# Kernel optimization log

Measured on AMD Instinct MI355X. Metric: run time of the kernel, lower is better.

## Reference

```python
import jax, jax.numpy as jnp
import numpy as np

HEADS = 16

def setup_inputs() -> dict:
    key = jax.random.key(0)
    ks = jax.random.split(key, 5)
    B, T, D = 4, 2048, 1024
    scale = 0.02
    return {
        "x": jax.random.normal(ks[0], (B, T, D), dtype=jnp.float32),
        "W_attn": jax.random.normal(ks[1], (D, 3 * D), dtype=jnp.float32) * scale,
        "b_attn": jax.random.normal(ks[2], (3 * D,), dtype=jnp.float32) * scale,
        "W_proj": jax.random.normal(ks[3], (D, D), dtype=jnp.float32) * scale,
        "b_proj": jax.random.normal(ks[4], (D,), dtype=jnp.float32) * scale,
    }

def reference(x, W_attn, b_attn, W_proj, b_proj):
    B, T, D = x.shape
    H = HEADS
    hd = D // H
    qkv = x @ W_attn + b_attn                      # [B, T, 3D]
    q, k, v = jnp.split(qkv, 3, axis=2)
    # [B, T, H, hd] -> [B, H, T, hd]
    q = q.reshape(B, T, H, hd).transpose(0, 2, 1, 3)
    k = k.reshape(B, T, H, hd).transpose(0, 2, 1, 3)
    v = v.reshape(B, T, H, hd).transpose(0, 2, 1, 3)
    scale = hd ** 0.5
    scores = jnp.einsum("bhqd,bhkd->bhqk", q, k) / scale
    causal = jnp.tril(jnp.ones((T, T), dtype=bool))
    scores = jnp.where(causal, scores, -jnp.inf)
    attn = jax.nn.softmax(scores, axis=-1)
    out = jnp.einsum("bhqk,bhkd->bhqd", attn, v)    # [B, H, T, hd]
    out = out.transpose(0, 2, 1, 3).reshape(B, T, D)
    return out @ W_proj + b_proj
```

## Files before the change

kernel.cpp:

```cpp
#include <hip/hip_runtime.h>
#include <hip/hip_bf16.h>

using bf16 = __hip_bfloat16;
typedef __attribute__((ext_vector_type(8))) __bf16 bf16x8;
typedef __attribute__((ext_vector_type(4))) short s16x4;
typedef __attribute__((ext_vector_type(4))) float f32x4;

#define B_   4
#define T_   2048
#define D_   1024
#define H_   16
#define HD_  64
#define BH_  (B_ * H_)
#define BT_  (B_ * T_)

#define QSCALE 0.18033688011112042f

__device__ __forceinline__ void gld_lds16(const void* g, void* l) {
    __builtin_amdgcn_global_load_lds(
        (const __attribute__((address_space(1))) unsigned int*)g,
        (__attribute__((address_space(3))) unsigned int*)l,
        16, 0, 0);
}

__device__ __forceinline__ f32x4 mfma16(s16x4 a, s16x4 b, f32x4 c) {
#if defined(__HIP_DEVICE_COMPILE__)
  #if __has_builtin(__builtin_amdgcn_mfma_f32_16x16x16bf16_1k)
    return __builtin_amdgcn_mfma_f32_16x16x16bf16_1k(a, b, c, 0, 0, 0);
  #else
    f32x4 d;
    asm volatile("v_mfma_f32_16x16x16_bf16 %0, %1, %2, %3\n\ts_nop 7\n\ts_nop 7"
                 : "=v"(d) : "v"(a), "v"(b), "v"(c));
    return d;
  #endif
#else
    (void)a; (void)b;
    return c;
#endif
}

__device__ __forceinline__ unsigned bfbits(float x) {
    return (unsigned)__builtin_bit_cast(unsigned short, __float2bfloat16(x));
}

__global__ void cast_kernel(const float* __restrict__ in, bf16* __restrict__ out, int n4) {
    int i = blockIdx.x * 256 + threadIdx.x;
    if (i >= n4) return;
    float4 v = reinterpret_cast<const float4*>(in)[i];
    union { bf16 h[4]; uint2 u; } tmp;
    tmp.h[0] = __float2bfloat16(v.x);
    tmp.h[1] = __float2bfloat16(v.y);
    tmp.h[2] = __float2bfloat16(v.z);
    tmp.h[3] = __float2bfloat16(v.w);
    reinterpret_cast<uint2*>(out)[i] = tmp.u;
}

__global__ void transpose_cast(const float* __restrict__ W, bf16* __restrict__ Wt,
                               int K, int N) {
    __shared__ float tile[32][33];
    int nb = blockIdx.x * 32, kb = blockIdx.y * 32;
    int tx = threadIdx.x, ty = threadIdx.y;
    #pragma unroll
    for (int i = 0; i < 32; i += 8)
        tile[ty + i][tx] = W[(size_t)(kb + ty + i) * N + nb + tx];
    __syncthreads();
    #pragma unroll
    for (int i = 0; i < 32; i += 8)
        Wt[(size_t)(nb + ty + i) * K + kb + tx] = __float2bfloat16(tile[tx][ty + i]);
}

template <int MODE>
__global__ __launch_bounds__(256)
void gemm_bt(const bf16* __restrict__ A, const bf16* __restrict__ Bt,
             const float* __restrict__ bias,
             bf16* __restrict__ Qo, bf16* __restrict__ Ko, bf16* __restrict__ Vo,
             float* __restrict__ Fo) {
    constexpr int K = 1024;
    const int bm = blockIdx.x * 128;
    const int bn = blockIdx.y * 128;
    const int tid  = threadIdx.x;
    const int wid  = tid >> 6;
    const int lane = tid & 63;
    const int wr = (wid >> 1) * 64;
    const int wc = (wid & 1) * 64;
    const int ln_g = lane >> 4;
    const int ln_c = lane & 15;

    __shared__ bf16 sm[3][2][128][32];

    f32x4 acc[4][4] = {};

    const int g_row0 = wid * 32 + (lane >> 2);
    const int g_chk  = ((lane & 3) ^ ((lane >> 3) & 3)) * 8;
    const int l_row0 = wid * 32;
    const int colx = (ln_g * 16) ^ (((ln_c >> 1) & 3) << 4);

#define STAGE(S_, K0_) {                                                              \
    gld_lds16(&A [(size_t)(bm + g_row0)      * K + (K0_) + g_chk], &sm[S_][0][l_row0][0]);      \
    gld_lds16(&A [(size_t)(bm + g_row0 + 16) * K + (K0_) + g_chk], &sm[S_][0][l_row0 + 16][0]); \
    gld_lds16(&Bt[(size_t)(bn + g_row0)      * K + (K0_) + g_chk], &sm[S_][1][l_row0][0]);      \
    gld_lds16(&Bt[(size_t)(bn + g_row0 + 16) * K + (K0_) + g_chk], &sm[S_][1][l_row0 + 16][0]); }

#define COMPUTE(S_) {                                                                    \
    bf16x8 af[4], bfr[4];                                                                \
    _Pragma("unroll")                                                                    \
    for (int m = 0; m < 4; ++m)                                                          \
        af[m] = *reinterpret_cast<const bf16x8*>(                                        \
            (const char*)&sm[S_][0][wr + m * 16 + ln_c][0] + colx);                      \
    _Pragma("unroll")                                                                    \
    for (int n = 0; n < 4; ++n)                                                          \
        bfr[n] = *reinterpret_cast<const bf16x8*>(                                       \
            (const char*)&sm[S_][1][wc + n * 16 + ln_c][0] + colx);                      \
    _Pragma("unroll")                                                                    \
    for (int m = 0; m < 4; ++m)                                                          \
        _Pragma("unroll")                                                                \
        for (int n = 0; n < 4; ++n)                                                      \
            acc[m][n] = __builtin_amdgcn_mfma_f32_16x16x32_bf16(af[m], bfr[n],           \
                                                                 acc[m][n], 0, 0, 0); }

#define WAITV4 { asm volatile("s_waitcnt vmcnt(4) lgkmcnt(0)" ::: "memory");             \
                 __builtin_amdgcn_s_barrier();                                           \
                 __builtin_amdgcn_sched_barrier(0); }
#define WAITV0 { asm volatile("s_waitcnt vmcnt(0) lgkmcnt(0)" ::: "memory");             \
                 __builtin_amdgcn_s_barrier();                                           \
                 __builtin_amdgcn_sched_barrier(0); }

    STAGE(0, 0);
    STAGE(1, 32);

    #pragma unroll 1
    for (int i = 0; i < 10; ++i) {
        const int kb = i * 96;
        WAITV4; STAGE(2, kb + 64);  COMPUTE(0);
        WAITV4; STAGE(0, kb + 96);  COMPUTE(1);
        WAITV4; STAGE(1, kb + 128); COMPUTE(2);
    }
    WAITV4; COMPUTE(0);
    WAITV0; COMPUTE(1);

#undef STAGE
#undef COMPUTE
#undef WAITV4
#undef WAITV0

    #pragma unroll
    for (int m = 0; m < 4; ++m) {
        #pragma unroll
        for (int n = 0; n < 4; ++n) {
            const int col = bn + wc + n * 16 + ln_c;
            const float bcol = bias[col];
            #pragma unroll
            for (int j = 0; j < 4; ++j) {
                const int row = bm + wr + m * 16 + ln_g * 4 + j;
                float v = acc[m][n][j] + bcol;
                if (MODE == 0) {
                    const int part = col >> 10;
                    const int cc = col & 1023;
                    const int h = cc >> 6, d = cc & 63;
                    const int b = row >> 11, t = row & 2047;
                    const int bh = b * H_ + h;
                    if (part == 0)
                        Qo[((size_t)bh * T_ + t) * HD_ + d] = __float2bfloat16(v * QSCALE);
                    else if (part == 1)
                        Ko[((size_t)bh * T_ + t) * HD_ + d] = __float2bfloat16(v);
                    else
                        Vo[((size_t)bh * HD_ + d) * T_ + t] = __float2bfloat16(v);
                } else {
                    Fo[(size_t)row * D_ + col] = v;
                }
            }
        }
    }
}

__global__ __launch_bounds__(256, 4)
void attn_kernel(const bf16* __restrict__ Q, const bf16* __restrict__ K,
                 const bf16* __restrict__ Vt, bf16* __restrict__ ctx) {
    const int bh = blockIdx.x & 63;
    const int qt = 31 - (blockIdx.x >> 6);
    const int tid  = threadIdx.x;
    const int wave = tid >> 6;
    const int lane = tid & 63;
    const int ln_g = lane >> 4;
    const int ln_c = lane & 15;

    const bf16* Qp = Q  + (size_t)bh * T_ * HD_;
    const bf16* Kp = K  + (size_t)bh * T_ * HD_;
    const bf16* Vp = Vt + (size_t)bh * HD_ * T_;

    __shared__ bf16 Ks[64][72];
    __shared__ bf16 Vs[64][72];

    const int srow = tid >> 3;
    const int sc8  = (tid & 7) * 8;

    const int b = bh >> 4, h = bh & 15;

    const int qbase = qt * 64;
    const int qglob = qbase + wave * 16 + ln_c;

    const bf16x8 qf0 = *reinterpret_cast<const bf16x8*>(&Qp[(size_t)qglob * HD_ + ln_g * 8]);
    const bf16x8 qf1 = *reinterpret_cast<const bf16x8*>(&Qp[(size_t)qglob * HD_ + 32 + ln_g * 8]);

    f32x4 o[4] = {};
    float m = -INFINITY, l = 0.f;

    const int nk = qt + 1;

    int4 kr0, kr1, vr0, vr1;
    kr0 = *reinterpret_cast<const int4*>(&Kp[(size_t)srow * HD_ + sc8]);
    kr1 = *reinterpret_cast<const int4*>(&Kp[(size_t)(srow + 32) * HD_ + sc8]);
    vr0 = *reinterpret_cast<const int4*>(&Vp[(size_t)srow * T_ + sc8]);
    vr1 = *reinterpret_cast<const int4*>(&Vp[(size_t)(srow + 32) * T_ + sc8]);
    *reinterpret_cast<int4*>(&Ks[srow][sc8])      = kr0;
    *reinterpret_cast<int4*>(&Ks[srow + 32][sc8]) = kr1;
    *reinterpret_cast<int4*>(&Vs[srow][sc8])      = vr0;
    *reinterpret_cast<int4*>(&Vs[srow + 32][sc8]) = vr1;
    __syncthreads();

    for (int it = 0; it < nk; ++it) {
        const int kb = it * 64;
        const bool notlast = (it + 1 < nk);
        if (notlast) {
            const int kn = kb + 64;
            kr0 = *reinterpret_cast<const int4*>(&Kp[(size_t)(kn + srow) * HD_ + sc8]);
            kr1 = *reinterpret_cast<const int4*>(&Kp[(size_t)(kn + srow + 32) * HD_ + sc8]);
            vr0 = *reinterpret_cast<const int4*>(&Vp[(size_t)srow * T_ + kn + sc8]);
            vr1 = *reinterpret_cast<const int4*>(&Vp[(size_t)(srow + 32) * T_ + kn + sc8]);
        }

        f32x4 st[4];
        __builtin_amdgcn_s_setprio(1);
        #pragma unroll
        for (int kk = 0; kk < 4; ++kk) {
            bf16x8 kfa = *reinterpret_cast<const bf16x8*>(&Ks[kk * 16 + ln_c][ln_g * 8]);
            bf16x8 kfb = *reinterpret_cast<const bf16x8*>(&Ks[kk * 16 + ln_c][32 + ln_g * 8]);
            f32x4 z = {0.f, 0.f, 0.f, 0.f};
            z = __builtin_amdgcn_mfma_f32_16x16x32_bf16(kfa, qf0, z, 0, 0, 0);
            z = __builtin_amdgcn_mfma_f32_16x16x32_bf16(kfb, qf1, z, 0, 0, 0);
            st[kk] = z;
        }
        __builtin_amdgcn_s_setprio(0);

        if (!notlast) {
            #pragma unroll
            for (int kk = 0; kk < 4; ++kk)
                #pragma unroll
                for (int j = 0; j < 4; ++j)
                    if (kb + kk * 16 + ln_g * 4 + j > qglob) st[kk][j] = -INFINITY;
        }

        float mx = -INFINITY;
        #pragma unroll
        for (int kk = 0; kk < 4; ++kk)
            #pragma unroll
            for (int j = 0; j < 4; ++j)
                mx = fmaxf(mx, st[kk][j]);
        if (!__all(mx - m <= 8.f)) {
            float r = fmaxf(mx, __shfl_xor(mx, 16));
            r = fmaxf(r, __shfl_xor(r, 32));
            const float mnew = fmaxf(m, r);
            const float alpha = exp2f(m - mnew);
            l *= alpha;
            #pragma unroll
            for (int dt = 0; dt < 4; ++dt)
                #pragma unroll
                for (int j = 0; j < 4; ++j)
                    o[dt][j] *= alpha;
            m = mnew;
        }

        #pragma unroll
        for (int kk = 0; kk < 4; ++kk) {
            float p0 = exp2f(st[kk][0] - m);
            float p1 = exp2f(st[kk][1] - m);
            float p2 = exp2f(st[kk][2] - m);
            float p3 = exp2f(st[kk][3] - m);
            l += (p0 + p1) + (p2 + p3);
            uint2 pw;
            pw.x = bfbits(p0) | (bfbits(p1) << 16);
            pw.y = bfbits(p2) | (bfbits(p3) << 16);
            const s16x4 ps = __builtin_bit_cast(s16x4, pw);
            __builtin_amdgcn_s_setprio(1);
            #pragma unroll
            for (int dt = 0; dt < 4; ++dt) {
                s16x4 vf = *reinterpret_cast<const s16x4*>(
                    &Vs[dt * 16 + ln_c][kk * 16 + ln_g * 4]);
                o[dt] = mfma16(vf, ps, o[dt]);
            }
            __builtin_amdgcn_s_setprio(0);
        }

        if (notlast) {
            __syncthreads();
            *reinterpret_cast<int4*>(&Ks[srow][sc8])      = kr0;
            *reinterpret_cast<int4*>(&Ks[srow + 32][sc8]) = kr1;
            *reinterpret_cast<int4*>(&Vs[srow][sc8])      = vr0;
            *reinterpret_cast<int4*>(&Vs[srow + 32][sc8]) = vr1;
            __syncthreads();
        }
    }

    l += __shfl_xor(l, 16);
    l += __shfl_xor(l, 32);
    const float inv = 1.0f / l;
    bf16* dst = ctx + ((size_t)(b * T_ + qglob)) * D_ + h * HD_;
    #pragma unroll
    for (int dt = 0; dt < 4; ++dt) {
        union { bf16 hh[4]; uint2 u; } ok;
        #pragma unroll
        for (int j = 0; j < 4; ++j)
            ok.hh[j] = __float2bfloat16(o[dt][j] * inv);
        *reinterpret_cast<uint2*>(&dst[dt * 16 + ln_g * 4]) = ok.u;
    }
}

extern "C" void kernel_launch(void* const* d_in, const int* in_sizes, int n_in,
                              void* d_out, int out_size, void* d_ws, size_t ws_size,
                              hipStream_t stream) {
    const float* x      = (const float*)d_in[0];
    const float* W_attn = (const float*)d_in[1];
    const float* b_attn = (const float*)d_in[2];
    const float* W_proj = (const float*)d_in[3];
    const float* b_proj = (const float*)d_in[4];
    float* out = (float*)d_out;

    char* ws = (char*)d_ws;
    bf16* xh  = (bf16*)ws;  ws += (size_t)BT_ * D_ * 2;
    bf16* WaT = (bf16*)ws;  ws += (size_t)3 * D_ * D_ * 2;
    bf16* WpT = (bf16*)ws;  ws += (size_t)D_ * D_ * 2;
    bf16* Qb  = (bf16*)ws;  ws += (size_t)BH_ * T_ * HD_ * 2;
    bf16* Kb  = (bf16*)ws;  ws += (size_t)BH_ * T_ * HD_ * 2;
    bf16* Vb  = (bf16*)ws;  ws += (size_t)BH_ * T_ * HD_ * 2;
    bf16* ctx = (bf16*)ws;  ws += (size_t)BT_ * D_ * 2;

    cast_kernel<<<(BT_ * D_ / 4 + 255) / 256, 256, 0, stream>>>(x, xh, BT_ * D_ / 4);
    transpose_cast<<<dim3(3 * D_ / 32, D_ / 32), dim3(32, 8), 0, stream>>>(W_attn, WaT, D_, 3 * D_);
    transpose_cast<<<dim3(D_ / 32, D_ / 32), dim3(32, 8), 0, stream>>>(W_proj, WpT, D_, D_);

    gemm_bt<0><<<dim3(BT_ / 128, 3 * D_ / 128), 256, 0, stream>>>(
        xh, WaT, b_attn, Qb, Kb, Vb, nullptr);

    attn_kernel<<<dim3(BH_ * 32), 256, 0, stream>>>(Qb, Kb, Vb, ctx);

    gemm_bt<1><<<dim3(BT_ / 128, D_ / 128), 256, 0, stream>>>(
        ctx, WpT, b_proj, nullptr, nullptr, nullptr, out);
}
```

Baseline: 186.2 us.

## Load GEMM A operand directly from global into registers, stage only B in LDS

The GEMM main loop stops staging the A tile through shared memory. Each wave now loads its A fragments straight from global memory into registers, double-buffered across iterations, while only B goes through a 4-deep LDS ring. The aim is to cut LDS traffic, LDS reads and shared-memory footprint, which could raise occupancy. In exchange, A rows are read from global with non-coalesced 16-byte strided loads, and the two column-waves load the same A rows twice, adding L2 traffic and extra register pressure.

```diff
diff --git a/kernel.cpp b/kernel.cpp
--- a/kernel.cpp
+++ b/kernel.cpp
@@ -86,7 +86,7 @@
     const int ln_g = lane >> 4;
     const int ln_c = lane & 15;
 
-    __shared__ bf16 sm[3][2][128][32];
+    __shared__ bf16 smB[4][128][32];
 
     f32x4 acc[4][4] = {};
 
@@ -95,53 +95,59 @@
     const int l_row0 = wid * 32;
     const int colx = (ln_g * 16) ^ (((ln_c >> 1) & 3) << 4);
 
-#define STAGE(S_, K0_) {                                                              \
-    gld_lds16(&A [(size_t)(bm + g_row0)      * K + (K0_) + g_chk], &sm[S_][0][l_row0][0]);      \
-    gld_lds16(&A [(size_t)(bm + g_row0 + 16) * K + (K0_) + g_chk], &sm[S_][0][l_row0 + 16][0]); \
-    gld_lds16(&Bt[(size_t)(bn + g_row0)      * K + (K0_) + g_chk], &sm[S_][1][l_row0][0]);      \
-    gld_lds16(&Bt[(size_t)(bn + g_row0 + 16) * K + (K0_) + g_chk], &sm[S_][1][l_row0 + 16][0]); }
-
-#define COMPUTE(S_) {                                                                    \
-    bf16x8 af[4], bfr[4];                                                                \
+    const bf16* Arow = A + (size_t)(bm + wr + ln_c) * K + ln_g * 8;
+
+#define LOADA(R_, T_) {                                                                  \
     _Pragma("unroll")                                                                    \
     for (int m = 0; m < 4; ++m)                                                          \
-        af[m] = *reinterpret_cast<const bf16x8*>(                                        \
-            (const char*)&sm[S_][0][wr + m * 16 + ln_c][0] + colx);                      \
+        R_[m] = *reinterpret_cast<const bf16x8*>(&Arow[(size_t)m * 16 * K + (T_) * 32]); }
+
+#define STAGEB(S_, T_) {                                                                 \
+    gld_lds16(&Bt[(size_t)(bn + g_row0)      * K + (T_) * 32 + g_chk], &smB[S_][l_row0][0]);      \
+    gld_lds16(&Bt[(size_t)(bn + g_row0 + 16) * K + (T_) * 32 + g_chk], &smB[S_][l_row0 + 16][0]); }
+
+#define COMPUTE(S_, AF_) {                                                               \
+    bf16x8 bfr[4];                                                                       \
     _Pragma("unroll")                                                                    \
     for (int n = 0; n < 4; ++n)                                                          \
         bfr[n] = *reinterpret_cast<const bf16x8*>(                                       \
-            (const char*)&sm[S_][1][wc + n * 16 + ln_c][0] + colx);                      \
+            (const char*)&smB[S_][wc + n * 16 + ln_c][0] + colx);                        \
     _Pragma("unroll")                                                                    \
     for (int m = 0; m < 4; ++m)                                                          \
         _Pragma("unroll")                                                                \
         for (int n = 0; n < 4; ++n)                                                      \
-            acc[m][n] = __builtin_amdgcn_mfma_f32_16x16x32_bf16(af[m], bfr[n],           \
+            acc[m][n] = __builtin_amdgcn_mfma_f32_16x16x32_bf16(AF_[m], bfr[n],          \
                                                                  acc[m][n], 0, 0, 0); }
 
-#define WAITV4 { asm volatile("s_waitcnt vmcnt(4) lgkmcnt(0)" ::: "memory");             \
-                 __builtin_amdgcn_s_barrier();                                           \
-                 __builtin_amdgcn_sched_barrier(0); }
-#define WAITV0 { asm volatile("s_waitcnt vmcnt(0) lgkmcnt(0)" ::: "memory");             \
-                 __builtin_amdgcn_s_barrier();                                           \
-                 __builtin_amdgcn_sched_barrier(0); }
-
-    STAGE(0, 0);
-    STAGE(1, 32);
+#define WAITV(N_) { asm volatile("s_waitcnt vmcnt(" #N_ ") lgkmcnt(0)" ::: "memory");    \
+                    __builtin_amdgcn_s_barrier();                                        \
+                    __builtin_amdgcn_sched_barrier(0); }
+
+    bf16x8 afA[4], afB[4];
+
+    STAGEB(0, 0);
+    STAGEB(1, 1);
+    STAGEB(2, 2);
+    LOADA(afA, 0);
+    WAITV(0);
 
     #pragma unroll 1
-    for (int i = 0; i < 10; ++i) {
-        const int kb = i * 96;
-        WAITV4; STAGE(2, kb + 64);  COMPUTE(0);
-        WAITV4; STAGE(0, kb + 96);  COMPUTE(1);
-        WAITV4; STAGE(1, kb + 128); COMPUTE(2);
+    for (int i = 0; i < 7; ++i) {
+        const int t0 = i * 4;
+        LOADA(afB, t0 + 1); STAGEB((t0 + 3) & 3, t0 + 3); COMPUTE((t0 + 0) & 3, afA); WAITV(2);
+        LOADA(afA, t0 + 2); STAGEB((t0 + 4) & 3, t0 + 4); COMPUTE((t0 + 1) & 3, afB); WAITV(2);
+        LOADA(afB, t0 + 3); STAGEB((t0 + 5) & 3, t0 + 5); COMPUTE((t0 + 2) & 3, afA); WAITV(2);
+        LOADA(afA, t0 + 4); STAGEB((t0 + 6) & 3, t0 + 6); COMPUTE((t0 + 3) & 3, afB); WAITV(2);
     }
-    WAITV4; COMPUTE(0);
-    WAITV0; COMPUTE(1);
-
-#undef STAGE
+    LOADA(afB, 29); STAGEB(3, 31); COMPUTE(0, afA); WAITV(2);
+    LOADA(afA, 30);                COMPUTE(1, afB); WAITV(0);
+    LOADA(afB, 31);                COMPUTE(2, afA); WAITV(0);
+                                   COMPUTE(3, afB);
+
+#undef LOADA
+#undef STAGEB
 #undef COMPUTE
-#undef WAITV4
-#undef WAITV0
+#undef WAITV
 
     #pragma unroll
     for (int m = 0; m < 4; ++m) {
```

New measurement: 254.4 us. 1.37x slower.

## Use 256x256 tiles with 8 waves for the QKV projection GEMM

Applied to the files above, without the earlier changes.

Adds a dedicated QKV GEMM kernel that uses 256x256 output tiles, 512 threads and 96KB of dynamic LDS, with each wave computing a 128x64 sub-tile. The larger tile raises the arithmetic intensity per LDS byte and reduces global reloads of A and B compared with 128x128 tiles. The output projection keeps the old kernel with the template split out. In exchange the grid drops to 384 blocks, which risks poorer occupancy and wave quantization across the CUs, and the doubled accumulator count raises register pressure.

```diff
diff --git a/kernel.cpp b/kernel.cpp
--- a/kernel.cpp
+++ b/kernel.cpp
@@ -69,12 +69,107 @@
         Wt[(size_t)(nb + ty + i) * K + kb + tx] = __float2bfloat16(tile[tx][ty + i]);
 }
 
-template <int MODE>
+__global__ __launch_bounds__(512, 2)
+void gemm_qkv256(const bf16* __restrict__ A, const bf16* __restrict__ Bt,
+                 const float* __restrict__ bias,
+                 bf16* __restrict__ Qo, bf16* __restrict__ Ko, bf16* __restrict__ Vo) {
+    constexpr int K = 1024;
+    extern __shared__ char smem[];
+    const int bm = blockIdx.x * 256;
+    const int bn = blockIdx.y * 256;
+    const int tid  = threadIdx.x;
+    const int wid  = tid >> 6;
+    const int lane = tid & 63;
+    const int wr = (wid >> 2) * 128;
+    const int wc = (wid & 3) * 64;
+    const int ln_g = lane >> 4;
+    const int ln_c = lane & 15;
+
+    f32x4 acc[8][4] = {};
+
+    const int s_row = wid * 16 + (lane >> 2);
+    const int g_chk = ((lane & 3) ^ ((lane >> 3) & 3)) * 8;
+    const int l_off = wid * 1024;
+
+    const int colx = (ln_g * 16) ^ (((ln_c >> 1) & 3) << 4);
+    const char* aB = smem + (wr + ln_c) * 64 + colx;
+    const char* bB = smem + 16384 + (wc + ln_c) * 64 + colx;
+
+#define STAGE(S_, T_) {                                                                   \
+    gld_lds16(&A [(size_t)(bm + s_row)       * K + (T_) * 32 + g_chk], smem + (S_)*32768 + l_off);          \
+    gld_lds16(&A [(size_t)(bm + 128 + s_row) * K + (T_) * 32 + g_chk], smem + (S_)*32768 + 8192 + l_off);   \
+    gld_lds16(&Bt[(size_t)(bn + s_row)       * K + (T_) * 32 + g_chk], smem + (S_)*32768 + 16384 + l_off);  \
+    gld_lds16(&Bt[(size_t)(bn + 128 + s_row) * K + (T_) * 32 + g_chk], smem + (S_)*32768 + 24576 + l_off); }
+
+#define COMPUTE(S_) {                                                                    \
+    bf16x8 af[8], bfr[4];                                                                \
+    _Pragma("unroll")                                                                    \
+    for (int m = 0; m < 8; ++m)                                                          \
+        af[m] = *reinterpret_cast<const bf16x8*>(aB + (S_) * 32768 + m * 1024);          \
+    _Pragma("unroll")                                                                    \
+    for (int n = 0; n < 4; ++n)                                                          \
+        bfr[n] = *reinterpret_cast<const bf16x8*>(bB + (S_) * 32768 + n * 1024);         \
+    _Pragma("unroll")                                                                    \
+    for (int m = 0; m < 8; ++m)                                                          \
+        _Pragma("unroll")                                                                \
+        for (int n = 0; n < 4; ++n)                                                      \
+            acc[m][n] = __builtin_amdgcn_mfma_f32_16x16x32_bf16(af[m], bfr[n],           \
+                                                                 acc[m][n], 0, 0, 0); }
+
+#define WAITV4 { asm volatile("s_waitcnt vmcnt(4) lgkmcnt(0)" ::: "memory");             \
+                 __builtin_amdgcn_s_barrier();                                           \
+                 __builtin_amdgcn_sched_barrier(0); }
+#define WAITV0 { asm volatile("s_waitcnt vmcnt(0) lgkmcnt(0)" ::: "memory");             \
+                 __builtin_amdgcn_s_barrier();                                           \
+                 __builtin_amdgcn_sched_barrier(0); }
+
+    STAGE(0, 0);
+    STAGE(1, 1);
+
+    #pragma unroll 1
+    for (int i = 0; i < 10; ++i) {
+        const int t0 = i * 3;
+        WAITV4; STAGE(2, t0 + 2); COMPUTE(0);
+        WAITV4; STAGE(0, t0 + 3); COMPUTE(1);
+        WAITV4; STAGE(1, t0 + 4); COMPUTE(2);
+    }
+    WAITV4; COMPUTE(0);
+    WAITV0; COMPUTE(1);
+
+#undef STAGE
+#undef COMPUTE
+#undef WAITV4
+#undef WAITV0
+
+    #pragma unroll
+    for (int m = 0; m < 8; ++m) {
+        #pragma unroll
+        for (int n = 0; n < 4; ++n) {
+            const int col = bn + wc + n * 16 + ln_c;
+            const float bcol = bias[col];
+            #pragma unroll
+            for (int j = 0; j < 4; ++j) {
+                const int row = bm + wr + m * 16 + ln_g * 4 + j;
+                float v = acc[m][n][j] + bcol;
+                const int part = col >> 10;
+                const int cc = col & 1023;
+                const int h = cc >> 6, d = cc & 63;
+                const int b = row >> 11, t = row & 2047;
+                const int bh = b * H_ + h;
+                if (part == 0)
+                    Qo[((size_t)bh * T_ + t) * HD_ + d] = __float2bfloat16(v * QSCALE);
+                else if (part == 1)
+                    Ko[((size_t)bh * T_ + t) * HD_ + d] = __float2bfloat16(v);
+                else
+                    Vo[((size_t)bh * HD_ + d) * T_ + t] = __float2bfloat16(v);
+            }
+        }
+    }
+}
+
 __global__ __launch_bounds__(256)
-void gemm_bt(const bf16* __restrict__ A, const bf16* __restrict__ Bt,
-             const float* __restrict__ bias,
-             bf16* __restrict__ Qo, bf16* __restrict__ Ko, bf16* __restrict__ Vo,
-             float* __restrict__ Fo) {
+void gemm_proj(const bf16* __restrict__ A, const bf16* __restrict__ Bt,
+               const float* __restrict__ bias, float* __restrict__ Fo) {
     constexpr int K = 1024;
     const int bm = blockIdx.x * 128;
     const int bn = blockIdx.y * 128;
@@ -95,11 +190,11 @@
     const int l_row0 = wid * 32;
     const int colx = (ln_g * 16) ^ (((ln_c >> 1) & 3) << 4);
 
-#define STAGE(S_, K0_) {                                                              \
-    gld_lds16(&A [(size_t)(bm + g_row0)      * K + (K0_) + g_chk], &sm[S_][0][l_row0][0]);      \
-    gld_lds16(&A [(size_t)(bm + g_row0 + 16) * K + (K0_) + g_chk], &sm[S_][0][l_row0 + 16][0]); \
-    gld_lds16(&Bt[(size_t)(bn + g_row0)      * K + (K0_) + g_chk], &sm[S_][1][l_row0][0]);      \
-    gld_lds16(&Bt[(size_t)(bn + g_row0 + 16) * K + (K0_) + g_chk], &sm[S_][1][l_row0 + 16][0]); }
+#define STAGE(S_, T_) {                                                               \
+    gld_lds16(&A [(size_t)(bm + g_row0)      * K + (T_) * 32 + g_chk], &sm[S_][0][l_row0][0]);      \
+    gld_lds16(&A [(size_t)(bm + g_row0 + 16) * K + (T_) * 32 + g_chk], &sm[S_][0][l_row0 + 16][0]); \
+    gld_lds16(&Bt[(size_t)(bn + g_row0)      * K + (T_) * 32 + g_chk], &sm[S_][1][l_row0][0]);      \
+    gld_lds16(&Bt[(size_t)(bn + g_row0 + 16) * K + (T_) * 32 + g_chk], &sm[S_][1][l_row0 + 16][0]); }
 
 #define COMPUTE(S_) {                                                                    \
     bf16x8 af[4], bfr[4];                                                                \
@@ -126,14 +221,14 @@
                  __builtin_amdgcn_sched_barrier(0); }
 
     STAGE(0, 0);
-    STAGE(1, 32);
+    STAGE(1, 1);
 
     #pragma unroll 1
     for (int i = 0; i < 10; ++i) {
-        const int kb = i * 96;
-        WAITV4; STAGE(2, kb + 64);  COMPUTE(0);
-        WAITV4; STAGE(0, kb + 96);  COMPUTE(1);
-        WAITV4; STAGE(1, kb + 128); COMPUTE(2);
+        const int t0 = i * 3;
+        WAITV4; STAGE(2, t0 + 2); COMPUTE(0);
+        WAITV4; STAGE(0, t0 + 3); COMPUTE(1);
+        WAITV4; STAGE(1, t0 + 4); COMPUTE(2);
     }
     WAITV4; COMPUTE(0);
     WAITV0; COMPUTE(1);
@@ -152,22 +247,7 @@
             #pragma unroll
             for (int j = 0; j < 4; ++j) {
                 const int row = bm + wr + m * 16 + ln_g * 4 + j;
-                float v = acc[m][n][j] + bcol;
-                if (MODE == 0) {
-                    const int part = col >> 10;
-                    const int cc = col & 1023;
-                    const int h = cc >> 6, d = cc & 63;
-                    const int b = row >> 11, t = row & 2047;
-                    const int bh = b * H_ + h;
-                    if (part == 0)
-                        Qo[((size_t)bh * T_ + t) * HD_ + d] = __float2bfloat16(v * QSCALE);
-                    else if (part == 1)
-                        Ko[((size_t)bh * T_ + t) * HD_ + d] = __float2bfloat16(v);
-                    else
-                        Vo[((size_t)bh * HD_ + d) * T_ + t] = __float2bfloat16(v);
-                } else {
-                    Fo[(size_t)row * D_ + col] = v;
-                }
+                Fo[(size_t)row * D_ + col] = acc[m][n][j] + bcol;
             }
         }
     }
@@ -338,11 +418,9 @@
     transpose_cast<<<dim3(3 * D_ / 32, D_ / 32), dim3(32, 8), 0, stream>>>(W_attn, WaT, D_, 3 * D_);
     transpose_cast<<<dim3(D_ / 32, D_ / 32), dim3(32, 8), 0, stream>>>(W_proj, WpT, D_, D_);
 
-    gemm_bt<0><<<dim3(BT_ / 128, 3 * D_ / 128), 256, 0, stream>>>(
-        xh, WaT, b_attn, Qb, Kb, Vb, nullptr);
+    gemm_qkv256<<<dim3(32, 12), 512, 98304, stream>>>(xh, WaT, b_attn, Qb, Kb, Vb);
 
     attn_kernel<<<dim3(BH_ * 32), 256, 0, stream>>>(Qb, Kb, Vb, ctx);
 
-    gemm_bt<1><<<dim3(BT_ / 128, D_ / 128), 256, 0, stream>>>(
-        ctx, WpT, b_proj, nullptr, nullptr, nullptr, out);
-}
+    gemm_proj<<<dim3(64, 8), 256, 0, stream>>>(ctx, WpT, b_proj, out);
+}
```

After: 193.4 us. +3.9%, slower.
